# Optimization experiments

Hardware: AMD Instinct MI355X
Metric: run time of the kernel (lower is better)

## Reference

```python
import jax, jax.numpy as jnp
import numpy as np
from jax.ops import segment_sum

N = 100000   # nodes
E = 1600000  # edges
D = 128      # input feature dim
H = 128      # hidden dim
S = 64       # substructure ids
G = 512      # graphs in batch
EPS = 1e-5


def setup_inputs() -> dict:
    key = jax.random.key(0)
    ks = jax.random.split(key, 12)
    subst_ids = jax.random.randint(ks[0], (N,), 0, S)
    x = jax.random.normal(ks[1], (N, D), dtype=jnp.float32)
    # column 5 carries the integer substructure id, as in data.x[:, 5].long()
    x = x.at[:, 5].set(subst_ids.astype(jnp.float32))
    edge_index = jax.random.randint(ks[2], (2, E), 0, N)
    batch = jnp.sort(jax.random.randint(ks[3], (N,), 0, G))
    s = 0.05  # weight scale to keep activations sane
    return {
        "x": x,
        "edge_index": edge_index,
        "subst_ids": subst_ids,
        "batch": batch,
        "attn_w1": jax.random.normal(ks[4], (D, 64), jnp.float32) * s,
        "attn_b1": jnp.zeros((64,), jnp.float32),
        "attn_w2": jax.random.normal(ks[5], (64, 1), jnp.float32) * s,
        "conv_w0": jax.random.normal(ks[6], (D + 1, H), jnp.float32) * s,
        "conv_b0": jnp.zeros((H,), jnp.float32),
        "conv_w1": jax.random.normal(ks[7], (H, H), jnp.float32) * s,
        "conv_b1": jnp.zeros((H,), jnp.float32),
        "conv_w2": jax.random.normal(ks[8], (H, H), jnp.float32) * s,
        "conv_b2": jnp.zeros((H,), jnp.float32),
        "conv_w3": jax.random.normal(ks[9], (H, H), jnp.float32) * s,
        "conv_b3": jnp.zeros((H,), jnp.float32),
        "bn_gamma": jnp.ones((4, H), jnp.float32),
        "bn_beta": jnp.zeros((4, H), jnp.float32),
        "bn_rmean": jnp.zeros((4, H), jnp.float32),
        "bn_rvar": jnp.ones((4, H), jnp.float32),
        "head_w1": jax.random.normal(ks[10], (H, H // 2), jnp.float32) * s,
        "head_b1": jnp.zeros((H // 2,), jnp.float32),
        "head_w2": jax.random.normal(ks[11], (H // 2, 1), jnp.float32) * s,
        "head_b2": jnp.zeros((1,), jnp.float32),
    }


def _gcn_conv(x, src, dst, dinv, w, b):
    # PyG GCNConv with self-loops: out[dst] += d^-1/2_src d^-1/2_dst (xW)[src]
    h = x @ w                                   # [N, H]
    coef = dinv[src] * dinv[dst]                # [E]
    agg = segment_sum(h[src] * coef[:, None], dst, num_segments=N)
    agg = agg + h * (dinv * dinv)[:, None]      # self-loop term
    return agg + b


def reference(x, edge_index, subst_ids, batch,
              attn_w1, attn_b1, attn_w2,
              conv_w0, conv_b0, conv_w1, conv_b1, conv_w2, conv_b2, conv_w3, conv_b3,
              bn_gamma, bn_beta, bn_rmean, bn_rvar,
              head_w1, head_b1, head_w2, head_b2):
    # --- substructure attention ---
    ones_n = jnp.ones((N,), x.dtype)
    cnt = jnp.maximum(segment_sum(ones_n, subst_ids, num_segments=S), 1.0)
    subst_mean = segment_sum(x, subst_ids, num_segments=S) / cnt[:, None]  # [S, D]
    scores = jnp.tanh(subst_mean @ attn_w1 + attn_b1) @ attn_w2            # [S, 1]
    subst_attn = jax.nn.softmax(scores, axis=0)                            # [S, 1]
    atom_attn = subst_attn[subst_ids]                                      # [N, 1]
    h = jnp.concatenate([x, atom_attn], axis=1)                            # [N, D+1]

    # --- shared symmetric normalization (self-loops included) ---
    src, dst = edge_index[0], edge_index[1]
    deg = segment_sum(jnp.ones((E,), x.dtype), dst, num_segments=N) + 1.0
    dinv = jax.lax.rsqrt(deg)

    convs = [(conv_w0, conv_b0), (conv_w1, conv_b1), (conv_w2, conv_b2), (conv_w3, conv_b3)]
    for i, (w, b) in enumerate(convs):
        h = _gcn_conv(h, src, dst, dinv, w, b)
        # BatchNorm1d in eval mode
        h = (h - bn_rmean[i]) * jax.lax.rsqrt(bn_rvar[i] + EPS) * bn_gamma[i] + bn_beta[i]
        h = jax.nn.elu(h) if i < 3 else jax.nn.relu(h)
        # dropout p=0.3 is identity in inference

    # --- global mean pool over graphs ---
    gcnt = jnp.maximum(segment_sum(jnp.ones((N,), x.dtype), batch, num_segments=G), 1.0)
    pooled = segment_sum(h, batch, num_segments=G) / gcnt[:, None]         # [G, H]

    # --- prediction head (dropout off) ---
    z = jax.nn.elu(pooled @ head_w1 + head_b1)
    return z @ head_w2 + head_b2                                            # [G, 1]
```

## Files before the change

### kernel.cpp

```cpp
#include <hip/hip_runtime.h>
#include <cmath>

#define NN 100000
#define EE 1600000
#define DD 128
#define HH 128
#define SS 64
#define GG 512

#define NBE 782
#define EBK 196
#define EHS 800

typedef float f32x4 __attribute__((ext_vector_type(4)));
typedef short s16x8 __attribute__((ext_vector_type(8)));

constexpr size_t alignup(size_t x){ return (x + 255) & ~(size_t)255; }
constexpr size_t SZ_P16   = (size_t)NN*64*sizeof(unsigned);
constexpr size_t OFF_HW   = 0;
constexpr size_t OFF_H    = alignup(OFF_HW + SZ_P16);
constexpr size_t OFF_X16  = alignup(OFF_H + SZ_P16);
constexpr size_t OFF_CSRS = alignup(OFF_X16 + SZ_P16);
constexpr size_t OFF_ROW  = alignup(OFF_CSRS + (size_t)EE*4);
constexpr size_t OFF_DINV = alignup(OFF_ROW + (size_t)(NN+1)*4);
constexpr size_t OFF_SATT = alignup(OFF_DINV + (size_t)NN*4);
constexpr size_t OFF_GST  = alignup(OFF_SATT + 64*4);
constexpr size_t OFF_BH   = alignup(OFF_GST + 513*4);
constexpr size_t OFF_BO   = alignup(OFF_BH + (size_t)64*400*4);
constexpr size_t OFF_TOT  = alignup(OFF_BO + (size_t)64*400*4);
constexpr size_t OFF_ROW2 = alignup(OFF_TOT + 64*4);
constexpr size_t OFF_LIST = alignup(OFF_ROW2 + 65*4);
constexpr size_t OFF_W16  = alignup(OFF_LIST + (size_t)NN*4);
constexpr size_t OFF_EH   = alignup(OFF_W16 + (size_t)4*8192*4);
constexpr size_t OFF_EB   = alignup(OFF_EH + (size_t)EBK*EHS*4);
constexpr size_t OFF_ET   = alignup(OFF_EB + (size_t)EBK*EHS*4);
constexpr size_t OFF_EBASE= alignup(OFF_ET + EBK*4);
constexpr size_t OFF_EPK  = alignup(OFF_EBASE + 200*4);
constexpr size_t OFF_POOL = alignup(OFF_EPK + (size_t)EE*4);
constexpr size_t OFF_GSUM = alignup(OFF_POOL + (size_t)GG*HH*4);
constexpr size_t OFF_END  = alignup(OFF_GSUM + (size_t)SS*DD*4);
constexpr size_t ZERO_BEG   = OFF_POOL;
constexpr size_t ZERO_BYTES = OFF_END - OFF_POOL;

__device__ __forceinline__ unsigned pack2bf(float a, float b){
  unsigned ua = __float_as_uint(a); ua += 0x7fffu + ((ua >> 16) & 1u);
  unsigned ub = __float_as_uint(b); ub += 0x7fffu + ((ub >> 16) & 1u);
  return (ua >> 16) | (ub & 0xffff0000u);
}
__device__ __forceinline__ float bf_lo(unsigned u){ return __uint_as_float(u << 16); }
__device__ __forceinline__ float bf_hi(unsigned u){ return __uint_as_float(u & 0xffff0000u); }
__device__ __forceinline__ s16x8 as_s16x8(uint4 v){ union { uint4 u; s16x8 s; } x; x.u = v; return x.s; }

__global__ __launch_bounds__(256) void hist_kernel(const int* __restrict__ sid, int* __restrict__ bhist)
{
  __shared__ int h[64];
  int t = threadIdx.x, b = blockIdx.x;
  if (t < 64) h[t] = 0;
  __syncthreads();
  int n = b*256 + t;
  if (n < NN) atomicAdd(&h[sid[n]], 1);
  __syncthreads();
  if (t < 64) bhist[t*400 + b] = h[t];
}

__global__ __launch_bounds__(512) void offs_kernel(const int* __restrict__ bhist, int* __restrict__ boff2, int* __restrict__ tots)
{
  __shared__ int sh[512];
  int s = blockIdx.x, t = threadIdx.x;
  int v = (t < 391) ? bhist[s*400 + t] : 0;
  sh[t] = v;
  __syncthreads();
  for (int off = 1; off < 512; off <<= 1) {
    int u = (t >= off) ? sh[t - off] : 0;
    __syncthreads();
    sh[t] += u;
    __syncthreads();
  }
  if (t < 391) boff2[s*400 + t] = sh[t] - v;
  if (t == 511) tots[s] = sh[511];
}

__global__ __launch_bounds__(64) void base_kernel(const int* __restrict__ tots, int* __restrict__ row2)
{
  int l = threadIdx.x;
  int v = tots[l];
  int xv = v;
  #pragma unroll
  for (int off = 1; off < 64; off <<= 1) {
    int u = __shfl_up(xv, off, 64);
    if (l >= off) xv += u;
  }
  row2[l] = xv - v;
  if (l == 63) row2[64] = xv;
}

__global__ __launch_bounds__(256) void fill2_kernel(
    const int* __restrict__ sid, const int* __restrict__ row2,
    const int* __restrict__ boff2, unsigned* __restrict__ list)
{
  __shared__ int h[64];
  int t = threadIdx.x, b = blockIdx.x;
  if (t < 64) h[t] = 0;
  __syncthreads();
  int n = b*256 + t;
  if (n < NN) {
    int s = sid[n];
    int lr = atomicAdd(&h[s], 1);
    int pos = row2[s] + boff2[s*400 + b] + lr;
    list[pos] = ((unsigned)s << 24) | (unsigned)n;
  }
}

__global__ __launch_bounds__(256) void subst_sum(
    const unsigned* __restrict__ list, const float* __restrict__ x,
    float* __restrict__ gsum)
{
  int b = blockIdx.x, t = threadIdx.x;
  int lane = t & 63, w = t >> 6;
  const int per = (NN + 1023)/1024;
  const int q   = (per + 3)/4;
  int bend = min(b*per + per, NN);
  int beg = b*per + w*q;
  int end = min(bend, beg + q);
  if (beg >= end) return;
  int d0 = lane * 2;
  float ax = 0.f, ay = 0.f;
  int scur = (int)(list[beg] >> 24);
  int i = beg;
  for (; i + 4 <= end; i += 4) {
    unsigned u0 = list[i], u1 = list[i+1], u2 = list[i+2], u3 = list[i+3];
    float2 v0 = *(const float2*)(x + (size_t)(u0 & 0xffffffu)*DD + d0);
    float2 v1 = *(const float2*)(x + (size_t)(u1 & 0xffffffu)*DD + d0);
    float2 v2 = *(const float2*)(x + (size_t)(u2 & 0xffffffu)*DD + d0);
    float2 v3 = *(const float2*)(x + (size_t)(u3 & 0xffffffu)*DD + d0);
    int s0 = u0 >> 24, s1 = u1 >> 24, s2 = u2 >> 24, s3 = u3 >> 24;
    if (s0 != scur) { atomicAdd(&gsum[scur*DD + d0], ax); atomicAdd(&gsum[scur*DD + d0 + 1], ay); scur = s0; ax = 0.f; ay = 0.f; }
    ax += v0.x; ay += v0.y;
    if (s1 != scur) { atomicAdd(&gsum[scur*DD + d0], ax); atomicAdd(&gsum[scur*DD + d0 + 1], ay); scur = s1; ax = 0.f; ay = 0.f; }
    ax += v1.x; ay += v1.y;
    if (s2 != scur) { atomicAdd(&gsum[scur*DD + d0], ax); atomicAdd(&gsum[scur*DD + d0 + 1], ay); scur = s2; ax = 0.f; ay = 0.f; }
    ax += v2.x; ay += v2.y;
    if (s3 != scur) { atomicAdd(&gsum[scur*DD + d0], ax); atomicAdd(&gsum[scur*DD + d0 + 1], ay); scur = s3; ax = 0.f; ay = 0.f; }
    ax += v3.x; ay += v3.y;
  }
  for (; i < end; ++i) {
    unsigned u = list[i];
    float2 v = *(const float2*)(x + (size_t)(u & 0xffffffu)*DD + d0);
    int s = u >> 24;
    if (s != scur) { atomicAdd(&gsum[scur*DD + d0], ax); atomicAdd(&gsum[scur*DD + d0 + 1], ay); scur = s; ax = 0.f; ay = 0.f; }
    ax += v.x; ay += v.y;
  }
  atomicAdd(&gsum[scur*DD + d0],     ax);
  atomicAdd(&gsum[scur*DD + d0 + 1], ay);
}

__global__ __launch_bounds__(1024) void attn_kernel(
    const float* __restrict__ g_sum, const int* __restrict__ row2,
    const float* __restrict__ w1, const float* __restrict__ b1,
    const float* __restrict__ w2, float* __restrict__ subst_attn)
{
  __shared__ float smean[SS*130];
  __shared__ float sw1[8192];
  __shared__ float sc[SS];
  int t = threadIdx.x;
  for (int i = t; i < SS*DD; i += 1024) {
    int s = i >> 7, d = i & 127;
    float c = fmaxf((float)(row2[s+1] - row2[s]), 1.0f);
    smean[s*130 + d] = g_sum[i] / c;
  }
  for (int i = t; i < 8192; i += 1024) sw1[i] = w1[i];
  __syncthreads();

  int s = t >> 4, jq = t & 15;
  float a0 = 0, a1 = 0, a2 = 0, a3 = 0;
  #pragma unroll 4
  for (int d = 0; d < 128; ++d) {
    float m = smean[s*130 + d];
    a0 += m * sw1[d*64 + jq     ];
    a1 += m * sw1[d*64 + jq + 16];
    a2 += m * sw1[d*64 + jq + 32];
    a3 += m * sw1[d*64 + jq + 48];
  }
  float acc = tanhf(a0 + b1[jq     ]) * w2[jq     ]
            + tanhf(a1 + b1[jq + 16]) * w2[jq + 16]
            + tanhf(a2 + b1[jq + 32]) * w2[jq + 32]
            + tanhf(a3 + b1[jq + 48]) * w2[jq + 48];
  acc += __shfl_xor(acc, 1, 64);
  acc += __shfl_xor(acc, 2, 64);
  acc += __shfl_xor(acc, 4, 64);
  acc += __shfl_xor(acc, 8, 64);
  if (jq == 0) sc[s] = acc;
  __syncthreads();
  if (t < 64) {
    float score = sc[t];
    float m = -1e30f;
    for (int i = 0; i < SS; ++i) m = fmaxf(m, sc[i]);
    float e = expf(score - m);
    float sum = 0.0f;
    for (int i = 0; i < SS; ++i) sum += expf(sc[i] - m);
    subst_attn[t] = e / sum;
  }
}

__global__ __launch_bounds__(256) void ehist_kernel(const int* __restrict__ dst, int* __restrict__ ehist)
{
  __shared__ int h[EBK];
  int t = threadIdx.x, b = blockIdx.x;
  if (t < EBK) h[t] = 0;
  __syncthreads();
  #pragma unroll
  for (int ii = 0; ii < 8; ++ii) {
    int e = b*2048 + ii*256 + t;
    if (e < EE) atomicAdd(&h[dst[e] >> 9], 1);
  }
  __syncthreads();
  if (t < EBK) ehist[t*EHS + b] = h[t];
}

__global__ __launch_bounds__(1024) void eoffs_kernel(const int* __restrict__ ehist, int* __restrict__ eboff, int* __restrict__ etots)
{
  __shared__ int sh[1024];
  int s = blockIdx.x, t = threadIdx.x;
  int v = (t < NBE) ? ehist[s*EHS + t] : 0;
  sh[t] = v;
  __syncthreads();
  for (int off = 1; off < 1024; off <<= 1) {
    int u = (t >= off) ? sh[t - off] : 0;
    __syncthreads();
    sh[t] += u;
    __syncthreads();
  }
  if (t < NBE) eboff[s*EHS + t] = sh[t] - v;
  if (t == 1023) etots[s] = sh[1023];
}

__global__ __launch_bounds__(256) void ebase_kernel(const int* __restrict__ etots, int* __restrict__ ebase)
{
  __shared__ int sh[256];
  int t = threadIdx.x;
  int v = (t < EBK) ? etots[t] : 0;
  sh[t] = v;
  __syncthreads();
  for (int off = 1; off < 256; off <<= 1) {
    int u = (t >= off) ? sh[t - off] : 0;
    __syncthreads();
    sh[t] += u;
    __syncthreads();
  }
  if (t < EBK) ebase[t] = sh[t] - v;
  if (t == EBK-1) ebase[EBK] = sh[t];
}

__global__ __launch_bounds__(256) void escat_kernel(
    const int* __restrict__ src, const int* __restrict__ dst,
    const int* __restrict__ ebase, const int* __restrict__ eboff,
    unsigned* __restrict__ epk)
{
  __shared__ int h[EBK];
  int t = threadIdx.x, b = blockIdx.x;
  if (t < EBK) h[t] = 0;
  __syncthreads();
  #pragma unroll
  for (int ii = 0; ii < 8; ++ii) {
    int e = b*2048 + ii*256 + t;
    if (e < EE) {
      int d = dst[e];
      int k = d >> 9;
      int lr = atomicAdd(&h[k], 1);
      int pos = ebase[k] + eboff[k*EHS + b] + lr;
      epk[pos] = ((unsigned)(d & 511) << 17) | (unsigned)src[e];
    }
  }
}

__global__ __launch_bounds__(1024) void csr_build(
    const int* __restrict__ ebase, const unsigned* __restrict__ epk,
    int* __restrict__ row_off, float* __restrict__ dinv, int* __restrict__ csr_src)
{
  __shared__ int scnt[512];
  __shared__ int sh[512];
  __shared__ int cur[512];
  int b = blockIdx.x, t = threadIdx.x;
  int base = ebase[b], cnt_b = ebase[b+1] - base;
  if (t < 512) scnt[t] = 0;
  __syncthreads();
  for (int i = t; i < cnt_b; i += 1024)
    atomicAdd(&scnt[epk[base + i] >> 17], 1);
  __syncthreads();
  int orig = (t < 512) ? scnt[t] : 0;
  if (t < 512) sh[t] = orig;
  __syncthreads();
  for (int off = 1; off < 512; off <<= 1) {
    int u = (t < 512 && t >= off) ? sh[t - off] : 0;
    __syncthreads();
    if (t < 512) sh[t] += u;
    __syncthreads();
  }
  if (t < 512) {
    int excl = sh[t] - orig;
    int n = b*512 + t;
    if (n < NN) {
      row_off[n] = base + excl;
      dinv[n] = rsqrtf((float)(orig + 1));
    }
    cur[t] = excl;
  }
  if (b == EBK-1 && t == 0) row_off[NN] = EE;
  __syncthreads();
  for (int i = t; i < cnt_b; i += 1024) {
    unsigned en = epk[base + i];
    int dl = en >> 17;
    int pos = atomicAdd(&cur[dl], 1);
    csr_src[base + pos] = (int)(en & 0x1FFFFu);
  }
}

__global__ __launch_bounds__(256) void packx_kernel(const float* __restrict__ x, unsigned* __restrict__ x16)
{
  int q = blockIdx.x*256 + threadIdx.x;
  const float4* xf = (const float4*)x;
  float4 f0 = xf[q*2], f1 = xf[q*2+1];
  uint4 pk;
  pk.x = pack2bf(f0.x, f0.y);
  pk.y = pack2bf(f0.z, f0.w);
  pk.z = pack2bf(f1.x, f1.y);
  pk.w = pack2bf(f1.z, f1.w);
  *(uint4*)(x16 + (size_t)q*4) = pk;
}

__global__ __launch_bounds__(256) void packw_kernel(const float* __restrict__ W, unsigned* __restrict__ W16)
{
  int q = blockIdx.x*256 + threadIdx.x;
  int c = q & 127, kp = q >> 7;
  float f0 = W[(size_t)(2*kp  )*128 + c];
  float f1 = W[(size_t)(2*kp+1)*128 + c];
  W16[c*64 + kp] = pack2bf(f0, f1);
}

__global__ __launch_bounds__(256) void gemm16_kernel(
    const unsigned* __restrict__ A16, const unsigned* __restrict__ W16,
    unsigned* __restrict__ out,
    const int* __restrict__ sid, const float* __restrict__ sattn,
    const float* __restrict__ wextra, int layer0)
{
  __shared__ unsigned lds[16384];
  __shared__ float sAttn[128];
  __shared__ float sExtra[128];
  int tid = threadIdx.x;
  int lane = tid & 63;
  int row0 = blockIdx.x * 128;

  if (layer0 && tid < 128) {
    int n = row0 + tid;
    sAttn[tid]  = (n < NN) ? sattn[sid[n]] : 0.0f;
    sExtra[tid] = wextra[tid];
  }

  #pragma unroll
  for (int p = 0; p < 8; ++p) {
    int q  = tid + 256*p;
    int r  = q >> 4;
    int ch = q & 15;
    int n = row0 + r;
    uint4 v = make_uint4(0u,0u,0u,0u);
    if (n < NN) v = *(const uint4*)(A16 + (size_t)n*64 + ch*4);
    int idx = (r*64 + ch*4) ^ ((r & 7) << 2);
    *(uint4*)&lds[idx] = v;
  }
  {
    const uint4* w4 = (const uint4*)W16;
    #pragma unroll
    for (int p = 0; p < 8; ++p) {
      int ch = tid + 256*p;
      int base = ch*4;
      int c = base >> 6;
      int idx = 8192 + (base ^ ((c & 7) << 2));
      *(uint4*)&lds[idx] = w4[ch];
    }
  }
  __syncthreads();

  int w = tid >> 6;
  int wrow = w * 32;
  int swz = (lane & 7) << 2;
  int kgrp = (lane >> 4) * 4;

  f32x4 acc0[8], acc1[8];
  #pragma unroll
  for (int j = 0; j < 8; ++j) { acc0[j] = (f32x4){0,0,0,0}; acc1[j] = (f32x4){0,0,0,0}; }

  #pragma unroll
  for (int kk = 0; kk < 4; ++kk) {
    int kbase = kk*16 + kgrp;
    int rowA0 = wrow + (lane & 15);
    int rowA1 = wrow + 16 + (lane & 15);
    uint4 avu0 = *(const uint4*)&lds[(rowA0*64 + kbase) ^ swz];
    uint4 avu1 = *(const uint4*)&lds[(rowA1*64 + kbase) ^ swz];
    s16x8 a0 = as_s16x8(avu0);
    s16x8 a1 = as_s16x8(avu1);
    #pragma unroll
    for (int j = 0; j < 8; ++j) {
      int col = j*16 + (lane & 15);
      uint4 bvu = *(const uint4*)&lds[8192 + ((col*64 + kbase) ^ swz)];
      s16x8 bfr = as_s16x8(bvu);
      acc0[j] = __builtin_amdgcn_mfma_f32_16x16x32_bf16(a0, bfr, acc0[j], 0, 0, 0);
      acc1[j] = __builtin_amdgcn_mfma_f32_16x16x32_bf16(a1, bfr, acc1[j], 0, 0, 0);
    }
  }
  __syncthreads();

  #pragma unroll
  for (int i2 = 0; i2 < 2; ++i2) {
    #pragma unroll
    for (int j = 0; j < 8; ++j) {
      f32x4 v = i2 ? acc1[j] : acc0[j];
      #pragma unroll
      for (int reg = 0; reg < 4; ++reg) {
        float own = v[reg];
        int r  = wrow + i2*16 + (lane >> 4)*4 + reg;
        if (layer0) {
          int col = j*16 + (lane & 15);
          own += sAttn[r] * sExtra[col];
        }
        float part = __shfl_xor(own, 1, 64);
        if ((lane & 1) == 0) {
          int cp = j*8 + ((lane & 15) >> 1);
          lds[r*68 + cp] = pack2bf(own, part);
        }
      }
    }
  }
  __syncthreads();

  #pragma unroll
  for (int p = 0; p < 8; ++p) {
    int q  = tid + 256*p;
    int r  = q >> 4;
    int ch = q & 15;
    int n = row0 + r;
    if (n < NN) {
      uint4 v = *(const uint4*)&lds[r*68 + ch*4];
      *(uint4*)(out + (size_t)n*64 + ch*4) = v;
    }
  }
}

__global__ __launch_bounds__(256) void gather_kernel(
    const unsigned* __restrict__ hw, const int* __restrict__ row_off,
    const int* __restrict__ csr_src,
    const float* __restrict__ dinv, const float* __restrict__ bias,
    const float* __restrict__ gma, const float* __restrict__ bta,
    const float* __restrict__ rmn, const float* __restrict__ rvr,
    unsigned* __restrict__ out, int relu_act)
{
  int w = (blockIdx.x*256 + threadIdx.x) >> 6;
  int lane = threadIdx.x & 63;
  int n0 = w * 2;
  if (n0 >= NN) return;
  n0 = __builtin_amdgcn_readfirstlane(n0);
  int n1 = n0 + 1;
  int j0 = lane * 2;

  float di0 = dinv[n0], di1 = dinv[n1];
  unsigned su0 = hw[(size_t)n0*64 + lane];
  unsigned su1 = hw[(size_t)n1*64 + lane];
  float ax0 = bf_lo(su0)*di0*di0, ay0 = bf_hi(su0)*di0*di0;
  float ax1 = bf_lo(su1)*di1*di1, ay1 = bf_hi(su1)*di1*di1;

  int b0 = __builtin_amdgcn_readfirstlane(row_off[n0]);
  int e0 = __builtin_amdgcn_readfirstlane(row_off[n0+1]);
  int e1 = __builtin_amdgcn_readfirstlane(row_off[n1+1]);
  int i0 = b0, i1 = e0;

  for (; i0 + 4 <= e0 && i1 + 4 <= e1; i0 += 4, i1 += 4) {
    int s00 = csr_src[i0+0], s01 = csr_src[i0+1], s02 = csr_src[i0+2], s03 = csr_src[i0+3];
    int s10 = csr_src[i1+0], s11 = csr_src[i1+1], s12 = csr_src[i1+2], s13 = csr_src[i1+3];
    unsigned u00 = hw[(size_t)s00*64 + lane];
    unsigned u01 = hw[(size_t)s01*64 + lane];
    unsigned u02 = hw[(size_t)s02*64 + lane];
    unsigned u03 = hw[(size_t)s03*64 + lane];
    unsigned u10 = hw[(size_t)s10*64 + lane];
    unsigned u11 = hw[(size_t)s11*64 + lane];
    unsigned u12 = hw[(size_t)s12*64 + lane];
    unsigned u13 = hw[(size_t)s13*64 + lane];
    float c00 = dinv[s00]*di0, c01 = dinv[s01]*di0, c02 = dinv[s02]*di0, c03 = dinv[s03]*di0;
    float c10 = dinv[s10]*di1, c11 = dinv[s11]*di1, c12 = dinv[s12]*di1, c13 = dinv[s13]*di1;
    ax0 += bf_lo(u00)*c00 + bf_lo(u01)*c01 + bf_lo(u02)*c02 + bf_lo(u03)*c03;
    ay0 += bf_hi(u00)*c00 + bf_hi(u01)*c01 + bf_hi(u02)*c02 + bf_hi(u03)*c03;
    ax1 += bf_lo(u10)*c10 + bf_lo(u11)*c11 + bf_lo(u12)*c12 + bf_lo(u13)*c13;
    ay1 += bf_hi(u10)*c10 + bf_hi(u11)*c11 + bf_hi(u12)*c12 + bf_hi(u13)*c13;
  }
  for (; i0 + 4 <= e0; i0 += 4) {
    int s0 = csr_src[i0+0], s1 = csr_src[i0+1], s2 = csr_src[i0+2], s3 = csr_src[i0+3];
    unsigned u0 = hw[(size_t)s0*64 + lane];
    unsigned u1 = hw[(size_t)s1*64 + lane];
    unsigned u2 = hw[(size_t)s2*64 + lane];
    unsigned u3 = hw[(size_t)s3*64 + lane];
    float c0 = dinv[s0]*di0, c1 = dinv[s1]*di0, c2 = dinv[s2]*di0, c3 = dinv[s3]*di0;
    ax0 += bf_lo(u0)*c0 + bf_lo(u1)*c1 + bf_lo(u2)*c2 + bf_lo(u3)*c3;
    ay0 += bf_hi(u0)*c0 + bf_hi(u1)*c1 + bf_hi(u2)*c2 + bf_hi(u3)*c3;
  }
  for (; i1 + 4 <= e1; i1 += 4) {
    int s0 = csr_src[i1+0], s1 = csr_src[i1+1], s2 = csr_src[i1+2], s3 = csr_src[i1+3];
    unsigned u0 = hw[(size_t)s0*64 + lane];
    unsigned u1 = hw[(size_t)s1*64 + lane];
    unsigned u2 = hw[(size_t)s2*64 + lane];
    unsigned u3 = hw[(size_t)s3*64 + lane];
    float c0 = dinv[s0]*di1, c1 = dinv[s1]*di1, c2 = dinv[s2]*di1, c3 = dinv[s3]*di1;
    ax1 += bf_lo(u0)*c0 + bf_lo(u1)*c1 + bf_lo(u2)*c2 + bf_lo(u3)*c3;
    ay1 += bf_hi(u0)*c0 + bf_hi(u1)*c1 + bf_hi(u2)*c2 + bf_hi(u3)*c3;
  }
  for (; i0 < e0; ++i0) {
    int s = csr_src[i0];
    float c = dinv[s]*di0;
    unsigned u = hw[(size_t)s*64 + lane];
    ax0 += bf_lo(u)*c; ay0 += bf_hi(u)*c;
  }
  for (; i1 < e1; ++i1) {
    int s = csr_src[i1];
    float c = dinv[s]*di1;
    unsigned u = hw[(size_t)s*64 + lane];
    ax1 += bf_lo(u)*c; ay1 += bf_hi(u)*c;
  }

  float iv0 = rsqrtf(rvr[j0]   + 1e-5f);
  float iv1 = rsqrtf(rvr[j0+1] + 1e-5f);
  float g0 = gma[j0], g1 = gma[j0+1];
  float m0 = rmn[j0], m1 = rmn[j0+1];
  float t0 = bta[j0], t1 = bta[j0+1];
  float bb0 = bias[j0], bb1 = bias[j0+1];

  float y00 = (ax0 + bb0 - m0) * iv0 * g0 + t0;
  float y01 = (ay0 + bb1 - m1) * iv1 * g1 + t1;
  float y10 = (ax1 + bb0 - m0) * iv0 * g0 + t0;
  float y11 = (ay1 + bb1 - m1) * iv1 * g1 + t1;
  if (relu_act) {
    y00 = fmaxf(y00, 0.0f); y01 = fmaxf(y01, 0.0f);
    y10 = fmaxf(y10, 0.0f); y11 = fmaxf(y11, 0.0f);
  } else {
    y00 = (y00 > 0.0f) ? y00 : expm1f(y00);
    y01 = (y01 > 0.0f) ? y01 : expm1f(y01);
    y10 = (y10 > 0.0f) ? y10 : expm1f(y10);
    y11 = (y11 > 0.0f) ? y11 : expm1f(y11);
  }
  out[(size_t)n0*64 + lane] = pack2bf(y00, y01);
  out[(size_t)n1*64 + lane] = pack2bf(y10, y11);
}

__global__ __launch_bounds__(256) void gstart_kernel(const int* __restrict__ batch, int* __restrict__ start)
{
  int n = blockIdx.x*256 + threadIdx.x;
  if (n >= NN) return;
  int b  = batch[n];
  int bp = (n == 0) ? -1 : batch[n-1];
  for (int g = bp + 1; g <= b; ++g) start[g] = n;
  if (n == NN-1) {
    for (int g = b + 1; g <= GG; ++g) start[g] = NN;
  }
}

__global__ __launch_bounds__(256) void pool_kernel(
    const unsigned* __restrict__ h16, const int* __restrict__ batch, float* __restrict__ pooled)
{
  int wave = (blockIdx.x*256 + threadIdx.x) >> 6;
  int lane = threadIdx.x & 63;
  const int CH = 64;
  int beg = wave * CH;
  if (beg >= NN) return;
  int end = min(beg + CH, NN);
  int j0 = lane * 2;
  float ax = 0.f, ay = 0.f;
  int gcur = batch[beg];
  for (int n = beg; n < end; ++n) {
    int g = batch[n];
    if (g != gcur) {
      atomicAdd(&pooled[(size_t)gcur*128 + j0],     ax);
      atomicAdd(&pooled[(size_t)gcur*128 + j0 + 1], ay);
      ax = 0.f; ay = 0.f; gcur = g;
    }
    unsigned u = h16[(size_t)n*64 + lane];
    ax += bf_lo(u); ay += bf_hi(u);
  }
  atomicAdd(&pooled[(size_t)gcur*128 + j0],     ax);
  atomicAdd(&pooled[(size_t)gcur*128 + j0 + 1], ay);
}

__global__ __launch_bounds__(64) void head_kernel(
    const float* __restrict__ pooled, const int* __restrict__ start,
    const float* __restrict__ w1, const float* __restrict__ b1,
    const float* __restrict__ w2, const float* __restrict__ b2,
    float* __restrict__ out)
{
  __shared__ float p[128];
  int g = blockIdx.x;
  int t = threadIdx.x;
  float cnt = fmaxf((float)(start[g+1] - start[g]), 1.0f);
  p[t]      = pooled[(size_t)g*128 + t]      / cnt;
  p[t + 64] = pooled[(size_t)g*128 + t + 64] / cnt;
  __syncthreads();
  float a = 0.f;
  #pragma unroll 4
  for (int d = 0; d < 128; ++d) a += p[d] * w1[d*64 + t];
  float z = a + b1[t];
  z = (z > 0.f) ? z : expm1f(z);
  float v = z * w2[t];
  #pragma unroll
  for (int off = 32; off > 0; off >>= 1) v += __shfl_down(v, off, 64);
  if (t == 0) out[g] = v + b2[0];
}

extern "C" void kernel_launch(void* const* d_in, const int* in_sizes, int n_in,
                              void* d_out, int out_size, void* d_ws, size_t ws_size,
                              hipStream_t stream)
{
  const float* x        = (const float*)d_in[0];
  const int*   eidx     = (const int*)d_in[1];
  const int*   sid      = (const int*)d_in[2];
  const int*   batch    = (const int*)d_in[3];
  const float* attn_w1  = (const float*)d_in[4];
  const float* attn_b1  = (const float*)d_in[5];
  const float* attn_w2  = (const float*)d_in[6];
  const float* conv_w[4] = {(const float*)d_in[7], (const float*)d_in[9],
                            (const float*)d_in[11], (const float*)d_in[13]};
  const float* conv_b[4] = {(const float*)d_in[8], (const float*)d_in[10],
                            (const float*)d_in[12], (const float*)d_in[14]};
  const float* bn_gamma = (const float*)d_in[15];
  const float* bn_beta  = (const float*)d_in[16];
  const float* bn_rmean = (const float*)d_in[17];
  const float* bn_rvar  = (const float*)d_in[18];
  const float* head_w1  = (const float*)d_in[19];
  const float* head_b1  = (const float*)d_in[20];
  const float* head_w2  = (const float*)d_in[21];
  const float* head_b2  = (const float*)d_in[22];
  float* out = (float*)d_out;

  char* ws = (char*)d_ws;
  unsigned* hw16  = (unsigned*)(ws + OFF_HW);
  unsigned* h16   = (unsigned*)(ws + OFF_H);
  unsigned* x16   = (unsigned*)(ws + OFF_X16);
  int*   csr_src  = (int*)  (ws + OFF_CSRS);
  int*   row_off  = (int*)  (ws + OFF_ROW);
  float* dinv     = (float*)(ws + OFF_DINV);
  float* sattn    = (float*)(ws + OFF_SATT);
  int*   gstart   = (int*)  (ws + OFF_GST);
  int*   bhist    = (int*)  (ws + OFF_BH);
  int*   boff2    = (int*)  (ws + OFF_BO);
  int*   tots     = (int*)  (ws + OFF_TOT);
  int*   row2     = (int*)  (ws + OFF_ROW2);
  unsigned* list  = (unsigned*)(ws + OFF_LIST);
  unsigned* w16   = (unsigned*)(ws + OFF_W16);
  int*   ehist    = (int*)  (ws + OFF_EH);
  int*   eboff    = (int*)  (ws + OFF_EB);
  int*   etots    = (int*)  (ws + OFF_ET);
  int*   ebase    = (int*)  (ws + OFF_EBASE);
  unsigned* epk   = (unsigned*)(ws + OFF_EPK);
  float* pooled   = (float*)(ws + OFF_POOL);
  float* gsum     = (float*)(ws + OFF_GSUM);

  const int* e_src = eidx;
  const int* e_dst = eidx + EE;

  hipMemsetAsync(ws + ZERO_BEG, 0, ZERO_BYTES, stream);

  int nb256 = (NN + 255)/256;

  hist_kernel <<<nb256, 256, 0, stream>>>(sid, bhist);
  offs_kernel <<<64, 512, 0, stream>>>(bhist, boff2, tots);
  base_kernel <<<1, 64, 0, stream>>>(tots, row2);
  fill2_kernel<<<nb256, 256, 0, stream>>>(sid, row2, boff2, list);
  subst_sum   <<<1024, 256, 0, stream>>>(list, x, gsum);
  attn_kernel <<<1, 1024, 0, stream>>>(gsum, row2, attn_w1, attn_b1, attn_w2, sattn);

  ehist_kernel<<<NBE, 256, 0, stream>>>(e_dst, ehist);
  eoffs_kernel<<<EBK, 1024, 0, stream>>>(ehist, eboff, etots);
  ebase_kernel<<<1, 256, 0, stream>>>(etots, ebase);
  escat_kernel<<<NBE, 256, 0, stream>>>(e_src, e_dst, ebase, eboff, epk);
  csr_build   <<<EBK, 1024, 0, stream>>>(ebase, epk, row_off, dinv, csr_src);

  gstart_kernel<<<nb256, 256, 0, stream>>>(batch, gstart);

  packx_kernel<<<(NN*16)/256, 256, 0, stream>>>(x, x16);
  for (int L = 0; L < 4; ++L)
    packw_kernel<<<32, 256, 0, stream>>>(conv_w[L], w16 + (size_t)L*8192);

  int gemm_grid = (NN + 127)/128;
  int gat_grid  = ((NN/2)*64 + 255)/256;
  for (int L = 0; L < 4; ++L) {
    const unsigned* A = (L == 0) ? x16 : h16;
    gemm16_kernel<<<gemm_grid, 256, 0, stream>>>(A, w16 + (size_t)L*8192, hw16,
        sid, sattn, conv_w[0] + 128*128, (L == 0) ? 1 : 0);
    gather_kernel<<<gat_grid, 256, 0, stream>>>(hw16, row_off, csr_src, dinv,
        conv_b[L], bn_gamma + L*HH, bn_beta + L*HH, bn_rmean + L*HH, bn_rvar + L*HH,
        h16, (L == 3) ? 1 : 0);
  }

  int pool_waves  = (NN + 63)/64;
  int pool_blocks = (pool_waves + 3)/4;
  pool_kernel<<<pool_blocks, 256, 0, stream>>>(h16, batch, pooled);
  head_kernel<<<GG, 64, 0, stream>>>(pooled, gstart, head_w1, head_b1, head_w2, head_b2, out);
}
```

Before: 514.3 us.

## Fuse neighbor gather with next layer's GEMM, ping-ponging buffers

Adds a fused kernel that performs a layer's CSR aggregation, batchnorm and ELU for a 128-node tile, writes the tile to LDS, and multiplies it by the next layer's weight with MFMA, emitting the next pre-aggregation features. This removes the intermediate h write/read and three kernel launches between gather and GEMM. The gather phase now runs with 512-thread blocks over 128 rows each, which changes occupancy and load balancing for the latency-bound gather. Layer-0 and final-layer kernels are specialized, removing their runtime flags.

```diff
diff --git a/kernel.cpp b/kernel.cpp
--- a/kernel.cpp
+++ b/kernel.cpp
@@ -341,7 +341,7 @@
     const unsigned* __restrict__ A16, const unsigned* __restrict__ W16,
     unsigned* __restrict__ out,
     const int* __restrict__ sid, const float* __restrict__ sattn,
-    const float* __restrict__ wextra, int layer0)
+    const float* __restrict__ wextra)
 {
   __shared__ unsigned lds[16384];
   __shared__ float sAttn[128];
@@ -350,7 +350,7 @@
   int lane = tid & 63;
   int row0 = blockIdx.x * 128;
 
-  if (layer0 && tid < 128) {
+  if (tid < 128) {
     int n = row0 + tid;
     sAttn[tid]  = (n < NN) ? sattn[sid[n]] : 0.0f;
     sExtra[tid] = wextra[tid];
@@ -418,10 +418,8 @@
       for (int reg = 0; reg < 4; ++reg) {
         float own = v[reg];
         int r  = wrow + i2*16 + (lane >> 4)*4 + reg;
-        if (layer0) {
-          int col = j*16 + (lane & 15);
-          own += sAttn[r] * sExtra[col];
-        }
+        int col = j*16 + (lane & 15);
+        own += sAttn[r] * sExtra[col];
         float part = __shfl_xor(own, 1, 64);
         if ((lane & 1) == 0) {
           int cp = j*8 + ((lane & 15) >> 1);
@@ -445,13 +443,182 @@
   }
 }
 
+__global__ __launch_bounds__(512) void fusedgg_kernel(
+    const unsigned* __restrict__ hw, const int* __restrict__ row_off,
+    const int* __restrict__ csr_src, const float* __restrict__ dinv,
+    const float* __restrict__ bias,
+    const float* __restrict__ gma, const float* __restrict__ bta,
+    const float* __restrict__ rmn, const float* __restrict__ rvr,
+    const unsigned* __restrict__ W16, unsigned* __restrict__ out)
+{
+  __shared__ unsigned lds[16384];
+  int tid = threadIdx.x;
+  int wid = tid >> 6;
+  int lane = tid & 63;
+  int row0 = blockIdx.x * 128;
+
+  {
+    const uint4* w4 = (const uint4*)W16;
+    #pragma unroll
+    for (int p = 0; p < 4; ++p) {
+      int ch = tid + 512*p;
+      int base = ch*4;
+      int c = base >> 6;
+      int idx = 8192 + (base ^ ((c & 7) << 2));
+      *(uint4*)&lds[idx] = w4[ch];
+    }
+  }
+
+  int j0 = lane * 2;
+  float iv0 = rsqrtf(rvr[j0]   + 1e-5f);
+  float iv1 = rsqrtf(rvr[j0+1] + 1e-5f);
+  float g0 = gma[j0], g1 = gma[j0+1];
+  float m0 = rmn[j0], m1 = rmn[j0+1];
+  float t0v = bta[j0], t1v = bta[j0+1];
+  float bb0 = bias[j0], bb1 = bias[j0+1];
+
+  for (int it = 0; it < 8; ++it) {
+    int n0 = row0 + wid*16 + it*2;
+    if (n0 < NN) {
+      n0 = __builtin_amdgcn_readfirstlane(n0);
+      int n1 = n0 + 1;
+      float di0 = dinv[n0], di1 = dinv[n1];
+      unsigned su0 = hw[(size_t)n0*64 + lane];
+      unsigned su1 = hw[(size_t)n1*64 + lane];
+      float ax0 = bf_lo(su0)*di0*di0, ay0 = bf_hi(su0)*di0*di0;
+      float ax1 = bf_lo(su1)*di1*di1, ay1 = bf_hi(su1)*di1*di1;
+
+      int b0 = __builtin_amdgcn_readfirstlane(row_off[n0]);
+      int e0 = __builtin_amdgcn_readfirstlane(row_off[n0+1]);
+      int e1 = __builtin_amdgcn_readfirstlane(row_off[n1+1]);
+      int i0 = b0, i1 = e0;
+
+      for (; i0 + 4 <= e0 && i1 + 4 <= e1; i0 += 4, i1 += 4) {
+        int s00 = csr_src[i0+0], s01 = csr_src[i0+1], s02 = csr_src[i0+2], s03 = csr_src[i0+3];
+        int s10 = csr_src[i1+0], s11 = csr_src[i1+1], s12 = csr_src[i1+2], s13 = csr_src[i1+3];
+        unsigned u00 = hw[(size_t)s00*64 + lane];
+        unsigned u01 = hw[(size_t)s01*64 + lane];
+        unsigned u02 = hw[(size_t)s02*64 + lane];
+        unsigned u03 = hw[(size_t)s03*64 + lane];
+        unsigned u10 = hw[(size_t)s10*64 + lane];
+        unsigned u11 = hw[(size_t)s11*64 + lane];
+        unsigned u12 = hw[(size_t)s12*64 + lane];
+        unsigned u13 = hw[(size_t)s13*64 + lane];
+        float c00 = dinv[s00]*di0, c01 = dinv[s01]*di0, c02 = dinv[s02]*di0, c03 = dinv[s03]*di0;
+        float c10 = dinv[s10]*di1, c11 = dinv[s11]*di1, c12 = dinv[s12]*di1, c13 = dinv[s13]*di1;
+        ax0 += bf_lo(u00)*c00 + bf_lo(u01)*c01 + bf_lo(u02)*c02 + bf_lo(u03)*c03;
+        ay0 += bf_hi(u00)*c00 + bf_hi(u01)*c01 + bf_hi(u02)*c02 + bf_hi(u03)*c03;
+        ax1 += bf_lo(u10)*c10 + bf_lo(u11)*c11 + bf_lo(u12)*c12 + bf_lo(u13)*c13;
+        ay1 += bf_hi(u10)*c10 + bf_hi(u11)*c11 + bf_hi(u12)*c12 + bf_hi(u13)*c13;
+      }
+      for (; i0 + 4 <= e0; i0 += 4) {
+        int s0 = csr_src[i0+0], s1 = csr_src[i0+1], s2 = csr_src[i0+2], s3 = csr_src[i0+3];
+        unsigned u0 = hw[(size_t)s0*64 + lane];
+        unsigned u1 = hw[(size_t)s1*64 + lane];
+        unsigned u2 = hw[(size_t)s2*64 + lane];
+        unsigned u3 = hw[(size_t)s3*64 + lane];
+        float c0 = dinv[s0]*di0, c1 = dinv[s1]*di0, c2 = dinv[s2]*di0, c3 = dinv[s3]*di0;
+        ax0 += bf_lo(u0)*c0 + bf_lo(u1)*c1 + bf_lo(u2)*c2 + bf_lo(u3)*c3;
+        ay0 += bf_hi(u0)*c0 + bf_hi(u1)*c1 + bf_hi(u2)*c2 + bf_hi(u3)*c3;
+      }
+      for (; i1 + 4 <= e1; i1 += 4) {
+        int s0 = csr_src[i1+0], s1 = csr_src[i1+1], s2 = csr_src[i1+2], s3 = csr_src[i1+3];
+        unsigned u0 = hw[(size_t)s0*64 + lane];
+        unsigned u1 = hw[(size_t)s1*64 + lane];
+        unsigned u2 = hw[(size_t)s2*64 + lane];
+        unsigned u3 = hw[(size_t)s3*64 + lane];
+        float c0 = dinv[s0]*di1, c1 = dinv[s1]*di1, c2 = dinv[s2]*di1, c3 = dinv[s3]*di1;
+        ax1 += bf_lo(u0)*c0 + bf_lo(u1)*c1 + bf_lo(u2)*c2 + bf_lo(u3)*c3;
+        ay1 += bf_hi(u0)*c0 + bf_hi(u1)*c1 + bf_hi(u2)*c2 + bf_hi(u3)*c3;
+      }
+      for (; i0 < e0; ++i0) {
+        int s = csr_src[i0];
+        float c = dinv[s]*di0;
+        unsigned u = hw[(size_t)s*64 + lane];
+        ax0 += bf_lo(u)*c; ay0 += bf_hi(u)*c;
+      }
+      for (; i1 < e1; ++i1) {
+        int s = csr_src[i1];
+        float c = dinv[s]*di1;
+        unsigned u = hw[(size_t)s*64 + lane];
+        ax1 += bf_lo(u)*c; ay1 += bf_hi(u)*c;
+      }
+
+      float y00 = (ax0 + bb0 - m0) * iv0 * g0 + t0v;
+      float y01 = (ay0 + bb1 - m1) * iv1 * g1 + t1v;
+      float y10 = (ax1 + bb0 - m0) * iv0 * g0 + t0v;
+      float y11 = (ay1 + bb1 - m1) * iv1 * g1 + t1v;
+      y00 = (y00 > 0.0f) ? y00 : expm1f(y00);
+      y01 = (y01 > 0.0f) ? y01 : expm1f(y01);
+      y10 = (y10 > 0.0f) ? y10 : expm1f(y10);
+      y11 = (y11 > 0.0f) ? y11 : expm1f(y11);
+
+      int r0 = n0 - row0, r1 = r0 + 1;
+      lds[(r0*64 + lane) ^ ((r0 & 7) << 2)] = pack2bf(y00, y01);
+      lds[(r1*64 + lane) ^ ((r1 & 7) << 2)] = pack2bf(y10, y11);
+    }
+  }
+  __syncthreads();
+
+  int wrow = wid * 16;
+  int swz = (lane & 7) << 2;
+  int kgrp = (lane >> 4) * 4;
+
+  f32x4 acc0[8];
+  #pragma unroll
+  for (int j = 0; j < 8; ++j) acc0[j] = (f32x4){0,0,0,0};
+
+  #pragma unroll
+  for (int kk = 0; kk < 4; ++kk) {
+    int kbase = kk*16 + kgrp;
+    int rowA0 = wrow + (lane & 15);
+    uint4 avu0 = *(const uint4*)&lds[(rowA0*64 + kbase) ^ swz];
+    s16x8 a0 = as_s16x8(avu0);
+    #pragma unroll
+    for (int j = 0; j < 8; ++j) {
+      int col = j*16 + (lane & 15);
+      uint4 bvu = *(const uint4*)&lds[8192 + ((col*64 + kbase) ^ swz)];
+      s16x8 bfr = as_s16x8(bvu);
+      acc0[j] = __builtin_amdgcn_mfma_f32_16x16x32_bf16(a0, bfr, acc0[j], 0, 0, 0);
+    }
+  }
+  __syncthreads();
+
+  #pragma unroll
+  for (int j = 0; j < 8; ++j) {
+    #pragma unroll
+    for (int reg = 0; reg < 4; ++reg) {
+      float own = acc0[j][reg];
+      float part = __shfl_xor(own, 1, 64);
+      if ((lane & 1) == 0) {
+        int r  = wrow + (lane >> 4)*4 + reg;
+        int cp = j*8 + ((lane & 15) >> 1);
+        lds[r*68 + cp] = pack2bf(own, part);
+      }
+    }
+  }
+  __syncthreads();
+
+  #pragma unroll
+  for (int p = 0; p < 4; ++p) {
+    int q  = tid + 512*p;
+    int r  = q >> 4;
+    int ch = q & 15;
+    int n = row0 + r;
+    if (n < NN) {
+      uint4 v = *(const uint4*)&lds[r*68 + ch*4];
+      *(uint4*)(out + (size_t)n*64 + ch*4) = v;
+    }
+  }
+}
+
 __global__ __launch_bounds__(256) void gather_kernel(
     const unsigned* __restrict__ hw, const int* __restrict__ row_off,
     const int* __restrict__ csr_src,
     const float* __restrict__ dinv, const float* __restrict__ bias,
     const float* __restrict__ gma, const float* __restrict__ bta,
     const float* __restrict__ rmn, const float* __restrict__ rvr,
-    unsigned* __restrict__ out, int relu_act)
+    unsigned* __restrict__ out)
 {
   int w = (blockIdx.x*256 + threadIdx.x) >> 6;
   int lane = threadIdx.x & 63;
@@ -530,19 +697,10 @@
   float t0 = bta[j0], t1 = bta[j0+1];
   float bb0 = bias[j0], bb1 = bias[j0+1];
 
-  float y00 = (ax0 + bb0 - m0) * iv0 * g0 + t0;
-  float y01 = (ay0 + bb1 - m1) * iv1 * g1 + t1;
-  float y10 = (ax1 + bb0 - m0) * iv0 * g0 + t0;
-  float y11 = (ay1 + bb1 - m1) * iv1 * g1 + t1;
-  if (relu_act) {
-    y00 = fmaxf(y00, 0.0f); y01 = fmaxf(y01, 0.0f);
-    y10 = fmaxf(y10, 0.0f); y11 = fmaxf(y11, 0.0f);
-  } else {
-    y00 = (y00 > 0.0f) ? y00 : expm1f(y00);
-    y01 = (y01 > 0.0f) ? y01 : expm1f(y01);
-    y10 = (y10 > 0.0f) ? y10 : expm1f(y10);
-    y11 = (y11 > 0.0f) ? y11 : expm1f(y11);
-  }
+  float y00 = fmaxf((ax0 + bb0 - m0) * iv0 * g0 + t0, 0.0f);
+  float y01 = fmaxf((ay0 + bb1 - m1) * iv1 * g1 + t1, 0.0f);
+  float y10 = fmaxf((ax1 + bb0 - m0) * iv0 * g0 + t0, 0.0f);
+  float y11 = fmaxf((ay1 + bb1 - m1) * iv1 * g1 + t1, 0.0f);
   out[(size_t)n0*64 + lane] = pack2bf(y00, y01);
   out[(size_t)n1*64 + lane] = pack2bf(y10, y11);
 }
@@ -635,8 +793,8 @@
   float* out = (float*)d_out;
 
   char* ws = (char*)d_ws;
-  unsigned* hw16  = (unsigned*)(ws + OFF_HW);
-  unsigned* h16   = (unsigned*)(ws + OFF_H);
+  unsigned* buf0  = (unsigned*)(ws + OFF_HW);
+  unsigned* buf1  = (unsigned*)(ws + OFF_H);
   unsigned* x16   = (unsigned*)(ws + OFF_X16);
   int*   csr_src  = (int*)  (ws + OFF_CSRS);
   int*   row_off  = (int*)  (ws + OFF_ROW);
@@ -685,17 +843,26 @@
 
   int gemm_grid = (NN + 127)/128;
   int gat_grid  = ((NN/2)*64 + 255)/256;
-  for (int L = 0; L < 4; ++L) {
-    const unsigned* A = (L == 0) ? x16 : h16;
-    gemm16_kernel<<<gemm_grid, 256, 0, stream>>>(A, w16 + (size_t)L*8192, hw16,
-        sid, sattn, conv_w[0] + 128*128, (L == 0) ? 1 : 0);
-    gather_kernel<<<gat_grid, 256, 0, stream>>>(hw16, row_off, csr_src, dinv,
-        conv_b[L], bn_gamma + L*HH, bn_beta + L*HH, bn_rmean + L*HH, bn_rvar + L*HH,
-        h16, (L == 3) ? 1 : 0);
-  }
+
+  gemm16_kernel<<<gemm_grid, 256, 0, stream>>>(x16, w16, buf0,
+      sid, sattn, conv_w[0] + 128*128);
+
+  fusedgg_kernel<<<gemm_grid, 512, 0, stream>>>(buf0, row_off, csr_src, dinv,
+      conv_b[0], bn_gamma + 0*HH, bn_beta + 0*HH, bn_rmean + 0*HH, bn_rvar + 0*HH,
+      w16 + (size_t)1*8192, buf1);
+  fusedgg_kernel<<<gemm_grid, 512, 0, stream>>>(buf1, row_off, csr_src, dinv,
+      conv_b[1], bn_gamma + 1*HH, bn_beta + 1*HH, bn_rmean + 1*HH, bn_rvar + 1*HH,
+      w16 + (size_t)2*8192, buf0);
+  fusedgg_kernel<<<gemm_grid, 512, 0, stream>>>(buf0, row_off, csr_src, dinv,
+      conv_b[2], bn_gamma + 2*HH, bn_beta + 2*HH, bn_rmean + 2*HH, bn_rvar + 2*HH,
+      w16 + (size_t)3*8192, buf1);
+
+  gather_kernel<<<gat_grid, 256, 0, stream>>>(buf1, row_off, csr_src, dinv,
+      conv_b[3], bn_gamma + 3*HH, bn_beta + 3*HH, bn_rmean + 3*HH, bn_rvar + 3*HH,
+      buf0);
 
   int pool_waves  = (NN + 63)/64;
   int pool_blocks = (pool_waves + 3)/4;
-  pool_kernel<<<pool_blocks, 256, 0, stream>>>(h16, batch, pooled);
+  pool_kernel<<<pool_blocks, 256, 0, stream>>>(buf0, batch, pooled);
   head_kernel<<<GG, 64, 0, stream>>>(pooled, gstart, head_w1, head_b1, head_w2, head_b2, out);
 }
```

Measured after the change: 579.1 us. 1.13x slower.
